# Kernel tuning notes

Hardware: AMD Instinct MI355X
Metric: run time of the kernel (lower is better)

Reference implementation:

```python
import jax, jax.numpy as jnp
import numpy as np

B, L, DIM = 2, 2048, 768
NH, HD = 12, 64  # num_heads, head_dim; NH*HD == dim_attn == 768


def setup_inputs() -> dict:
    key = jax.random.key(0)
    ks = jax.random.split(key, 7)
    x = jax.random.normal(ks[0], (B, L, DIM), dtype=jnp.float32)
    pos_bias = jax.random.normal(ks[1], (1, NH, L, L), dtype=jnp.float32)
    Wq = jax.random.normal(ks[2], (DIM, DIM), dtype=jnp.float32) * 0.02
    Wk = jax.random.normal(ks[3], (DIM, DIM), dtype=jnp.float32) * 0.02
    Wv = jax.random.normal(ks[4], (DIM, DIM), dtype=jnp.float32) * 0.02
    Wo = jax.random.normal(ks[5], (DIM, DIM), dtype=jnp.float32) * 0.02
    mask = jax.random.randint(ks[6], (B, L), 0, 2, dtype=jnp.int32)
    return {"x": x, "pos_bias": pos_bias, "Wq": Wq, "Wk": Wk, "Wv": Wv,
            "Wo": Wo, "mask": mask}


def reference(x, pos_bias, Wq, Wk, Wv, Wo, mask):
    b, l, _ = x.shape
    # q/k/v projections (torch Linear: x @ W.T), split into heads
    q = (x @ Wq.T).reshape(b, l, NH, HD)
    k = (x @ Wk.T).reshape(b, l, NH, HD)
    v = (x @ Wv.T).reshape(b, l, NH, HD)
    # additive bias [B, H, Lq, Lk]: pos_bias broadcast + key mask -> -inf
    neg_inf = jnp.finfo(x.dtype).min
    attn_bias = jnp.broadcast_to(pos_bias, (b, NH, l, l))
    attn_bias = jnp.where(mask[:, None, None, :] == 0, neg_inf, attn_bias)
    # T5-style attention: NO 1/sqrt(d) scaling
    scores = jnp.einsum('binc,bjnc->bnij', q, k) + attn_bias
    attn = jax.nn.softmax(scores.astype(jnp.float32), axis=-1).astype(x.dtype)
    out = jnp.einsum('bnij,bjnc->binc', attn, v).reshape(b, l, NH * HD)
    return out @ Wo.T
```

## Files before the change

kernel.cpp:

```cpp
#include <hip/hip_runtime.h>
#include <math.h>

#define Bq 2
#define Lq 2048
#define DIMq 768
#define NHq 12
#define HDq 64
#define LOG2E 1.44269504f

typedef __attribute__((ext_vector_type(8))) short short8;
typedef __attribute__((ext_vector_type(4))) short short4v;
typedef __attribute__((ext_vector_type(4))) float float4v;

typedef __attribute__((address_space(3))) unsigned int as3_u32;
typedef __attribute__((address_space(1))) unsigned int as1_u32;

static __device__ __forceinline__ short f2bf(float f) {
    union { float f; unsigned u; } v; v.f = f;
    unsigned r = (v.u + 0x7FFF + ((v.u >> 16) & 1)) >> 16;
    return (short)r;
}

static __device__ __forceinline__ void gld_lds16(const short* g, short* l) {
    __builtin_amdgcn_global_load_lds((const as1_u32*)g, (as3_u32*)l, 16, 0, 0);
}

__global__ __launch_bounds__(256)
void to_bf16(const float* __restrict__ x,  const float* __restrict__ wq,
             const float* __restrict__ wk, const float* __restrict__ wv,
             const float* __restrict__ wo,
             short* __restrict__ xb, short* __restrict__ wqb,
             short* __restrict__ wkb, short* __restrict__ wvb,
             short* __restrict__ wob)
{
    int blk = blockIdx.x;
    const float* s; short* d; int off;
    if      (blk <  768) { s = x;  d = xb;  off = blk * 1024; }
    else if (blk <  912) { s = wq; d = wqb; off = (blk -  768) * 1024; }
    else if (blk < 1056) { s = wk; d = wkb; off = (blk -  912) * 1024; }
    else if (blk < 1200) { s = wv; d = wvb; off = (blk - 1056) * 1024; }
    else                 { s = wo; d = wob; off = (blk - 1200) * 1024; }
    const float4* s4 = (const float4*)s;
    short4v* d4 = (short4v*)d;
#pragma unroll
    for (int i = 0; i < 4; ++i) {
        int idx = off + threadIdx.x + i * 256;
        float4 v = s4[idx];
        short4v o;
        o[0] = f2bf(v.x); o[1] = f2bf(v.y); o[2] = f2bf(v.z); o[3] = f2bf(v.w);
        d4[idx] = o;
    }
}

__global__ __launch_bounds__(256, 2)
void gemm_bf16(const short* __restrict__ A,
               const short* __restrict__ W0, const short* __restrict__ W1,
               const short* __restrict__ W2,
               short* __restrict__ D0, short* __restrict__ D1,
               short* __restrict__ D2, float* __restrict__ DF, int mode)
{
    const int z = blockIdx.z;
    const short* W = (z == 0) ? W0 : ((z == 1) ? W1 : W2);
    short* DH = (z == 0) ? D0 : ((z == 1) ? D1 : D2);

    __shared__ __align__(16) short As[128][64];
    __shared__ __align__(16) short Ws[128][64];

    const int tid  = threadIdx.x;
    const int wave = tid >> 6;
    const int lane = tid & 63;
    const int col  = lane & 15;
    const int quad = lane >> 4;
    const int wr = wave >> 1, wc = wave & 1;
    const int m0 = blockIdx.y * 128, n0 = blockIdx.x * 128;

    float4v acc[4][4];
#pragma unroll
    for (int mt = 0; mt < 4; ++mt)
#pragma unroll
        for (int nt = 0; nt < 4; ++nt) acc[mt][nt] = (float4v){0.f, 0.f, 0.f, 0.f};

    const short* Ab = A + (size_t)m0 * DIMq;
    const short* Wb = W + (size_t)n0 * DIMq;

    for (int k0 = 0; k0 < DIMq; k0 += 64) {
        __syncthreads();
#pragma unroll
        for (int i = 0; i < 4; ++i) {
            int g = i * 256 + tid;
            int row = g >> 3, ch = g & 7;
            gld_lds16(Ab + (size_t)row * DIMq + k0 + ch * 8, (short*)As + g * 8);
            gld_lds16(Wb + (size_t)row * DIMq + k0 + ch * 8, (short*)Ws + g * 8);
        }
        __syncthreads();
#pragma unroll
        for (int kk = 0; kk < 2; ++kk) {
            short8 a[4], bfr[4];
#pragma unroll
            for (int mt = 0; mt < 4; ++mt)
                a[mt] = *(const short8*)&As[wr * 64 + mt * 16 + col][kk * 32 + quad * 8];
#pragma unroll
            for (int nt = 0; nt < 4; ++nt)
                bfr[nt] = *(const short8*)&Ws[wc * 64 + nt * 16 + col][kk * 32 + quad * 8];
#pragma unroll
            for (int mt = 0; mt < 4; ++mt)
#pragma unroll
                for (int nt = 0; nt < 4; ++nt)
                    acc[mt][nt] = __builtin_amdgcn_mfma_f32_16x16x32_bf16(
                        a[mt], bfr[nt], acc[mt][nt], 0, 0, 0);
        }
    }

#pragma unroll
    for (int mt = 0; mt < 4; ++mt)
#pragma unroll
    for (int reg = 0; reg < 4; ++reg) {
        int m = m0 + wr * 64 + mt * 16 + quad * 4 + reg;
#pragma unroll
        for (int nt = 0; nt < 4; ++nt) {
            int n = n0 + wc * 64 + nt * 16 + col;
            if (mode == 1) {
                int b = m >> 11, l = m & 2047, h = n >> 6, c = n & 63;
                DH[(((size_t)(b * NHq + h)) * Lq + l) * HDq + c] = f2bf(acc[mt][nt][reg]);
            } else {
                DF[(size_t)m * DIMq + n] = acc[mt][nt][reg];
            }
        }
    }
}

__global__ __launch_bounds__(256)
void transpose_v(const short* __restrict__ Vh, short* __restrict__ VT)
{
    const int lt = blockIdx.x;
    const int bh = blockIdx.y;
    const short* src = Vh + ((size_t)bh * Lq + lt * 64) * HDq;
    short* dst = VT + (size_t)bh * HDq * Lq + lt * 64;
    __shared__ __align__(16) short t[64][72];
    const int tid = threadIdx.x;
    {
        int row = tid & 63, seg = tid >> 6;
        *(short8*)&t[row][seg * 16]     = *(const short8*)&src[row * HDq + seg * 16];
        *(short8*)&t[row][seg * 16 + 8] = *(const short8*)&src[row * HDq + seg * 16 + 8];
    }
    __syncthreads();
    {
        int c = tid >> 2, seg = tid & 3;
        short8 o0, o1;
#pragma unroll
        for (int j = 0; j < 8; ++j) o0[j] = t[seg * 16 + j][c];
#pragma unroll
        for (int j = 0; j < 8; ++j) o1[j] = t[seg * 16 + 8 + j][c];
        *(short8*)&dst[(size_t)c * Lq + seg * 16]     = o0;
        *(short8*)&dst[(size_t)c * Lq + seg * 16 + 8] = o1;
    }
}

__global__ __launch_bounds__(256, 2)
void attn_fwd_mfma(const short* __restrict__ Qh, const short* __restrict__ Kh,
                   const short* __restrict__ VT, const float* __restrict__ pos_bias,
                   const int* __restrict__ mask, short* __restrict__ AO)
{
    const int hw = blockIdx.x;
    const int logical = (hw & 7) * 96 + (hw >> 3);
    const int b  = logical & 1;
    const int qt = (logical >> 1) & 31;
    const int h  = logical >> 6;

    const short* Q = Qh + ((size_t)(b * NHq + h)) * Lq * HDq;
    const short* K = Kh + ((size_t)(b * NHq + h)) * Lq * HDq;
    const short* V = VT + ((size_t)(b * NHq + h)) * HDq * Lq;
    const int* mk = mask + (size_t)b * Lq;

    __shared__ __align__(16) short Ks[2][64][72];
    __shared__ __align__(16) short Vt[2][64][72];
    __shared__ __align__(16) short Ps[64][72];

    const int tid  = threadIdx.x;
    const int wave = tid >> 6;
    const int lane = tid & 63;
    const int col  = lane & 15;
    const int quad = lane >> 4;

    short8 qa[2];
    {
        const short* qrow = Q + (size_t)(qt * 64 + wave * 16 + col) * HDq;
        qa[0] = *(const short8*)&qrow[quad * 8];
        qa[1] = *(const short8*)&qrow[32 + quad * 8];
    }

    const float* brow = pos_bias + (size_t)h * Lq * Lq
                      + (size_t)(qt * 64 + wave * 16 + quad * 4) * Lq + col;

    float bcur[4][4], bnxt[4][4];
    auto prefetch = [&](int kt, float (&bb)[4][4]) {
#pragma unroll
        for (int nt = 0; nt < 4; ++nt) {
            int mval = mk[kt * 64 + col + 16 * nt];
            float fm = (mval == 0) ? -1e30f : 0.0f;
#pragma unroll
            for (int reg = 0; reg < 4; ++reg)
                bb[nt][reg] = (brow[(size_t)reg * Lq + kt * 64 + 16 * nt] + fm) * LOG2E;
        }
    };

    short8 kreg[2], vreg[2];
    auto loadKV = [&](int kt) {
        const short* Kt = K + (size_t)kt * 64 * HDq;
#pragma unroll
        for (int i = 0; i < 2; ++i) {
            int idx = tid + i * 256;
            kreg[i] = *(const short8*)&Kt[(idx >> 3) * HDq + (idx & 7) * 8];
            vreg[i] = *(const short8*)&V[(size_t)(idx >> 3) * Lq + kt * 64 + (idx & 7) * 8];
        }
    };
    auto writeKV = [&](int buf) {
#pragma unroll
        for (int i = 0; i < 2; ++i) {
            int idx = tid + i * 256;
            *(short8*)&Ks[buf][idx >> 3][(idx & 7) * 8] = kreg[i];
            *(short8*)&Vt[buf][idx >> 3][(idx & 7) * 8] = vreg[i];
        }
    };

    float4v Oacc[4];
    float l_part[4];
#pragma unroll
    for (int nt = 0; nt < 4; ++nt) Oacc[nt] = (float4v){0.f, 0.f, 0.f, 0.f};
#pragma unroll
    for (int r = 0; r < 4; ++r) l_part[r] = 0.f;

    loadKV(0);
    writeKV(0);
    prefetch(0, bcur);
    __syncthreads();

    int cur = 0;
    for (int kt = 0; kt < Lq / 64; ++kt) {
        const bool more = (kt + 1 < Lq / 64);
        if (more) {
            loadKV(kt + 1);
            prefetch(kt + 1, bnxt);
        }

        float4v S[4];
#pragma unroll
        for (int nt = 0; nt < 4; ++nt) S[nt] = (float4v){0.f, 0.f, 0.f, 0.f};
        __builtin_amdgcn_s_setprio(1);
#pragma unroll
        for (int kk = 0; kk < 2; ++kk) {
#pragma unroll
            for (int nt = 0; nt < 4; ++nt) {
                short8 bfr = *(const short8*)&Ks[cur][nt * 16 + col][kk * 32 + quad * 8];
                S[nt] = __builtin_amdgcn_mfma_f32_16x16x32_bf16(qa[kk], bfr, S[nt], 0, 0, 0);
            }
        }
        __builtin_amdgcn_s_setprio(0);

#pragma unroll
        for (int nt = 0; nt < 4; ++nt)
#pragma unroll
            for (int reg = 0; reg < 4; ++reg) {
                float p = __builtin_amdgcn_exp2f(
                    __builtin_fmaf(S[nt][reg], LOG2E, bcur[nt][reg]));
                l_part[reg] += p;
                Ps[wave * 16 + quad * 4 + reg][col + 16 * nt] = f2bf(p);
            }

        __builtin_amdgcn_s_setprio(1);
#pragma unroll
        for (int kk = 0; kk < 2; ++kk) {
            short8 pa = *(const short8*)&Ps[wave * 16 + col][kk * 32 + quad * 8];
#pragma unroll
            for (int nt = 0; nt < 4; ++nt) {
                short8 vb = *(const short8*)&Vt[cur][nt * 16 + col][kk * 32 + quad * 8];
                Oacc[nt] = __builtin_amdgcn_mfma_f32_16x16x32_bf16(pa, vb, Oacc[nt], 0, 0, 0);
            }
        }
        __builtin_amdgcn_s_setprio(0);

        if (more) writeKV(cur ^ 1);
        __syncthreads();
        cur ^= 1;

#pragma unroll
        for (int nt = 0; nt < 4; ++nt)
#pragma unroll
            for (int reg = 0; reg < 4; ++reg)
                bcur[nt][reg] = bnxt[nt][reg];
    }

    float l[4];
#pragma unroll
    for (int reg = 0; reg < 4; ++reg) {
        float s = l_part[reg];
#pragma unroll
        for (int off = 1; off < 16; off <<= 1)
            s += __shfl_xor(s, off, 64);
        l[reg] = s;
    }

    short* aorow = AO + ((size_t)b * Lq + qt * 64 + wave * 16 + quad * 4) * DIMq
                 + h * HDq + col;
#pragma unroll
    for (int reg = 0; reg < 4; ++reg) {
        float inv = 1.0f / l[reg];
#pragma unroll
        for (int nt = 0; nt < 4; ++nt)
            aorow[(size_t)reg * DIMq + 16 * nt] = f2bf(Oacc[nt][reg] * inv);
    }
}

extern "C" void kernel_launch(void* const* d_in, const int* in_sizes, int n_in,
                              void* d_out, int out_size, void* d_ws, size_t ws_size,
                              hipStream_t stream) {
    const float* x        = (const float*)d_in[0];
    const float* pos_bias = (const float*)d_in[1];
    const float* Wq       = (const float*)d_in[2];
    const float* Wk       = (const float*)d_in[3];
    const float* Wv       = (const float*)d_in[4];
    const float* Wo       = (const float*)d_in[5];
    const int*   mask     = (const int*)d_in[6];
    float* out = (float*)d_out;

    const size_t nX = (size_t)Bq * Lq * DIMq;
    const size_t nW = (size_t)DIMq * DIMq;
    short* xb  = (short*)d_ws;
    short* wqb = xb  + nX;
    short* wkb = wqb + nW;
    short* wvb = wkb + nW;
    short* wob = wvb + nW;
    short* Qh  = wob + nW;
    short* Kh  = Qh  + nX;
    short* Vh  = Kh  + nX;
    short* AOb = Vh  + nX;
    short* VTb = xb;

    dim3 blk(256);
    hipLaunchKernelGGL(to_bf16, dim3(1344), blk, 0, stream,
                       x, Wq, Wk, Wv, Wo, xb, wqb, wkb, wvb, wob);

    hipLaunchKernelGGL(gemm_bf16, dim3(DIMq / 128, (Bq * Lq) / 128, 3), blk, 0, stream,
                       xb, wqb, wkb, wvb, Qh, Kh, Vh, (float*)nullptr, 1);

    hipLaunchKernelGGL(transpose_v, dim3(Lq / 64, Bq * NHq), blk, 0, stream,
                       Vh, VTb);

    hipLaunchKernelGGL(attn_fwd_mfma, dim3(Lq / 64 * NHq * Bq), blk, 0, stream,
                       Qh, Kh, VTb, pos_bias, mask, AOb);

    hipLaunchKernelGGL(gemm_bf16, dim3(DIMq / 128, (Bq * Lq) / 128, 1), blk, 0, stream,
                       AOb, wob, wob, wob, (short*)nullptr, (short*)nullptr,
                       (short*)nullptr, out, 0);
}
```

Measured before the change: 388.1 us.

## Split attention over key dimension and swizzle LDS tiles to avoid bank conflicts

The attention kernel now splits the key sequence into two halves, doubling the grid to 1536 blocks. Each block writes unnormalized fp32 partial outputs and row sums, and a new combine kernel adds the halves, normalizes and converts to bf16. This works without a running max because the kernel uses no max subtraction. The LDS tiles also drop padding in favour of an XOR swizzle, to reduce bank conflicts and shared memory use. The split raises parallelism and occupancy, at the cost of an extra launch and extra fp32 global traffic for the partials.

Result: slower. 400.4 us (+3.2%).

```diff
diff --git a/kernel.cpp b/kernel.cpp
--- a/kernel.cpp
+++ b/kernel.cpp
@@ -7,6 +7,8 @@
 #define NHq 12
 #define HDq 64
 #define LOG2E 1.44269504f
+#define NSPLIT 2
+#define KT_PER_SPLIT (Lq / 64 / NSPLIT)
 
 typedef __attribute__((ext_vector_type(8))) short short8;
 typedef __attribute__((ext_vector_type(4))) short short4v;
@@ -159,22 +161,24 @@
 __global__ __launch_bounds__(256, 2)
 void attn_fwd_mfma(const short* __restrict__ Qh, const short* __restrict__ Kh,
                    const short* __restrict__ VT, const float* __restrict__ pos_bias,
-                   const int* __restrict__ mask, short* __restrict__ AO)
+                   const int* __restrict__ mask,
+                   float* __restrict__ Op, float* __restrict__ Lp)
 {
     const int hw = blockIdx.x;
-    const int logical = (hw & 7) * 96 + (hw >> 3);
-    const int b  = logical & 1;
-    const int qt = (logical >> 1) & 31;
-    const int h  = logical >> 6;
+    const int logical = (hw & 7) * 192 + (hw >> 3);
+    const int s  = logical & 1;
+    const int b  = (logical >> 1) & 1;
+    const int qt = (logical >> 2) & 31;
+    const int h  = logical >> 7;
 
     const short* Q = Qh + ((size_t)(b * NHq + h)) * Lq * HDq;
     const short* K = Kh + ((size_t)(b * NHq + h)) * Lq * HDq;
     const short* V = VT + ((size_t)(b * NHq + h)) * HDq * Lq;
     const int* mk = mask + (size_t)b * Lq;
 
-    __shared__ __align__(16) short Ks[2][64][72];
-    __shared__ __align__(16) short Vt[2][64][72];
-    __shared__ __align__(16) short Ps[64][72];
+    __shared__ __align__(16) short Ks[2][64][64];
+    __shared__ __align__(16) short Vt[2][64][64];
+    __shared__ __align__(16) short Ps[64][64];
 
     const int tid  = threadIdx.x;
     const int wave = tid >> 6;
@@ -182,6 +186,9 @@
     const int col  = lane & 15;
     const int quad = lane >> 4;
 
+    const int ktbeg = s * KT_PER_SPLIT;
+    const int ktend = ktbeg + KT_PER_SPLIT;
+
     short8 qa[2];
     {
         const short* qrow = Q + (size_t)(qt * 64 + wave * 16 + col) * HDq;
@@ -218,8 +225,10 @@
 #pragma unroll
         for (int i = 0; i < 2; ++i) {
             int idx = tid + i * 256;
-            *(short8*)&Ks[buf][idx >> 3][(idx & 7) * 8] = kreg[i];
-            *(short8*)&Vt[buf][idx >> 3][(idx & 7) * 8] = vreg[i];
+            int row = idx >> 3;
+            int ofs = ((idx & 7) * 16) ^ ((row & 7) << 4);
+            *(short8*)((char*)&Ks[buf][0][0] + row * 128 + ofs) = kreg[i];
+            *(short8*)((char*)&Vt[buf][0][0] + row * 128 + ofs) = vreg[i];
         }
     };
 
@@ -230,19 +239,20 @@
 #pragma unroll
     for (int r = 0; r < 4; ++r) l_part[r] = 0.f;
 
-    loadKV(0);
+    loadKV(ktbeg);
     writeKV(0);
-    prefetch(0, bcur);
+    prefetch(ktbeg, bcur);
     __syncthreads();
 
     int cur = 0;
-    for (int kt = 0; kt < Lq / 64; ++kt) {
-        const bool more = (kt + 1 < Lq / 64);
+    for (int kt = ktbeg; kt < ktend; ++kt) {
+        const bool more = (kt + 1 < ktend);
         if (more) {
             loadKV(kt + 1);
             prefetch(kt + 1, bnxt);
         }
 
+        const int rofs = (col & 7) << 4;
         float4v S[4];
 #pragma unroll
         for (int nt = 0; nt < 4; ++nt) S[nt] = (float4v){0.f, 0.f, 0.f, 0.f};
@@ -251,7 +261,8 @@
         for (int kk = 0; kk < 2; ++kk) {
 #pragma unroll
             for (int nt = 0; nt < 4; ++nt) {
-                short8 bfr = *(const short8*)&Ks[cur][nt * 16 + col][kk * 32 + quad * 8];
+                short8 bfr = *(const short8*)((const char*)&Ks[cur][0][0]
+                              + (nt * 16 + col) * 128 + ((kk * 64 + quad * 16) ^ rofs));
                 S[nt] = __builtin_amdgcn_mfma_f32_16x16x32_bf16(qa[kk], bfr, S[nt], 0, 0, 0);
             }
         }
@@ -264,16 +275,20 @@
                 float p = __builtin_amdgcn_exp2f(
                     __builtin_fmaf(S[nt][reg], LOG2E, bcur[nt][reg]));
                 l_part[reg] += p;
-                Ps[wave * 16 + quad * 4 + reg][col + 16 * nt] = f2bf(p);
+                int prow = wave * 16 + quad * 4 + reg;
+                *(short*)((char*)&Ps[0][0] + prow * 128
+                          + (((col + 16 * nt) * 2) ^ ((prow & 7) << 4))) = f2bf(p);
             }
 
         __builtin_amdgcn_s_setprio(1);
 #pragma unroll
         for (int kk = 0; kk < 2; ++kk) {
-            short8 pa = *(const short8*)&Ps[wave * 16 + col][kk * 32 + quad * 8];
+            short8 pa = *(const short8*)((const char*)&Ps[0][0]
+                          + (wave * 16 + col) * 128 + ((kk * 64 + quad * 16) ^ rofs));
 #pragma unroll
             for (int nt = 0; nt < 4; ++nt) {
-                short8 vb = *(const short8*)&Vt[cur][nt * 16 + col][kk * 32 + quad * 8];
+                short8 vb = *(const short8*)((const char*)&Vt[cur][0][0]
+                              + (nt * 16 + col) * 128 + ((kk * 64 + quad * 16) ^ rofs));
                 Oacc[nt] = __builtin_amdgcn_mfma_f32_16x16x32_bf16(pa, vb, Oacc[nt], 0, 0, 0);
             }
         }
@@ -293,22 +308,52 @@
     float l[4];
 #pragma unroll
     for (int reg = 0; reg < 4; ++reg) {
-        float s = l_part[reg];
+        float v = l_part[reg];
 #pragma unroll
         for (int off = 1; off < 16; off <<= 1)
-            s += __shfl_xor(s, off, 64);
-        l[reg] = s;
-    }
-
-    short* aorow = AO + ((size_t)b * Lq + qt * 64 + wave * 16 + quad * 4) * DIMq
-                 + h * HDq + col;
-#pragma unroll
-    for (int reg = 0; reg < 4; ++reg) {
-        float inv = 1.0f / l[reg];
+            v += __shfl_xor(v, off, 64);
+        l[reg] = v;
+    }
+
+    float* orow = Op + (((size_t)(s * Bq + b)) * Lq + qt * 64 + wave * 16 + quad * 4) * DIMq
+                + h * HDq + col;
+#pragma unroll
+    for (int reg = 0; reg < 4; ++reg)
 #pragma unroll
         for (int nt = 0; nt < 4; ++nt)
-            aorow[(size_t)reg * DIMq + 16 * nt] = f2bf(Oacc[nt][reg] * inv);
-    }
+            orow[(size_t)reg * DIMq + 16 * nt] = Oacc[nt][reg];
+
+    if (col == 0) {
+        float* lrow = Lp + (((size_t)(s * Bq + b)) * NHq + h) * Lq
+                    + qt * 64 + wave * 16 + quad * 4;
+#pragma unroll
+        for (int reg = 0; reg < 4; ++reg) lrow[reg] = l[reg];
+    }
+}
+
+__global__ __launch_bounds__(256)
+void combine_split(const float* __restrict__ Op, const float* __restrict__ Lp,
+                   short* __restrict__ AO)
+{
+    const int idx = blockIdx.x * 256 + threadIdx.x;
+    const int row = idx / (DIMq / 4);
+    const int d4  = idx - row * (DIMq / 4);
+    const int h   = d4 >> 4;
+    const int b   = row >> 11, l = row & 2047;
+
+    const float4* O0 = (const float4*)Op;
+    const float4* O1 = O0 + (size_t)Bq * Lq * (DIMq / 4);
+    float l0 = Lp[((size_t)b * NHq + h) * Lq + l];
+    float l1 = Lp[(((size_t)Bq + b) * NHq + h) * Lq + l];
+    float inv = 1.0f / (l0 + l1);
+
+    float4 a = O0[idx], c = O1[idx];
+    short4v o;
+    o[0] = f2bf((a.x + c.x) * inv);
+    o[1] = f2bf((a.y + c.y) * inv);
+    o[2] = f2bf((a.z + c.z) * inv);
+    o[3] = f2bf((a.w + c.w) * inv);
+    ((short4v*)AO)[idx] = o;
 }
 
 extern "C" void kernel_launch(void* const* d_in, const int* in_sizes, int n_in,
@@ -334,6 +379,8 @@
     short* Kh  = Qh  + nX;
     short* Vh  = Kh  + nX;
     short* AOb = Vh  + nX;
+    float* Opf = (float*)(AOb + nX);
+    float* Lpf = Opf + (size_t)NSPLIT * nX;
     short* VTb = xb;
 
     dim3 blk(256);
@@ -346,8 +393,11 @@
     hipLaunchKernelGGL(transpose_v, dim3(Lq / 64, Bq * NHq), blk, 0, stream,
                        Vh, VTb);
 
-    hipLaunchKernelGGL(attn_fwd_mfma, dim3(Lq / 64 * NHq * Bq), blk, 0, stream,
-                       Qh, Kh, VTb, pos_bias, mask, AOb);
+    hipLaunchKernelGGL(attn_fwd_mfma, dim3(Lq / 64 * NHq * Bq * NSPLIT), blk, 0, stream,
+                       Qh, Kh, VTb, pos_bias, mask, Opf, Lpf);
+
+    hipLaunchKernelGGL(combine_split, dim3(nX / 4 / 256), blk, 0, stream,
+                       Opf, Lpf, AOb);
 
     hipLaunchKernelGGL(gemm_bf16, dim3(DIMq / 128, (Bq * Lq) / 128, 1), blk, 0, stream,
                        AOb, wob, wob, wob, (short*)nullptr, (short*)nullptr,
```

## Split attention key tiles across wave pairs with 512-thread blocks

Applied to the files above, without the earlier changes.

The attention kernel now runs 8 waves per block instead of 4. Each pair of waves shares a 16-row query slice and splits the 64-key tile (and the 64 output columns) in half, so each wave does half the MFMAs and half the bias loads. The goal is more parallelism and latency hiding for the bias streaming that dominates the kernel. This adds an extra __syncthreads per iteration, because P is written by both waves before the PV step, and a shared-memory exchange to combine the row sums at the end. Launch bounds rise to 512 threads with 6 blocks per CU, which caps registers per thread.

Result: no change. 384.1 us (-1.0%).

```diff
diff --git a/kernel.cpp b/kernel.cpp
--- a/kernel.cpp
+++ b/kernel.cpp
@@ -156,7 +156,7 @@
     }
 }
 
-__global__ __launch_bounds__(256, 2)
+__global__ __launch_bounds__(512, 6)
 void attn_fwd_mfma(const short* __restrict__ Qh, const short* __restrict__ Kh,
                    const short* __restrict__ VT, const float* __restrict__ pos_bias,
                    const int* __restrict__ mask, short* __restrict__ AO)
@@ -175,58 +175,55 @@
     __shared__ __align__(16) short Ks[2][64][72];
     __shared__ __align__(16) short Vt[2][64][72];
     __shared__ __align__(16) short Ps[64][72];
+    __shared__ float lbuf[8][16];
 
     const int tid  = threadIdx.x;
     const int wave = tid >> 6;
     const int lane = tid & 63;
     const int col  = lane & 15;
     const int quad = lane >> 4;
+    const int wrow = wave >> 1;
+    const int wkey = wave & 1;
 
     short8 qa[2];
     {
-        const short* qrow = Q + (size_t)(qt * 64 + wave * 16 + col) * HDq;
+        const short* qrow = Q + (size_t)(qt * 64 + wrow * 16 + col) * HDq;
         qa[0] = *(const short8*)&qrow[quad * 8];
         qa[1] = *(const short8*)&qrow[32 + quad * 8];
     }
 
     const float* brow = pos_bias + (size_t)h * Lq * Lq
-                      + (size_t)(qt * 64 + wave * 16 + quad * 4) * Lq + col;
-
-    float bcur[4][4], bnxt[4][4];
-    auto prefetch = [&](int kt, float (&bb)[4][4]) {
-#pragma unroll
-        for (int nt = 0; nt < 4; ++nt) {
-            int mval = mk[kt * 64 + col + 16 * nt];
+                      + (size_t)(qt * 64 + wrow * 16 + quad * 4) * Lq + col;
+
+    float bcur[2][4], bnxt[2][4];
+    auto prefetch = [&](int kt, float (&bb)[2][4]) {
+#pragma unroll
+        for (int ntl = 0; ntl < 2; ++ntl) {
+            int nt = wkey * 2 + ntl;
+            int mval = mk[kt * 64 + nt * 16 + col];
             float fm = (mval == 0) ? -1e30f : 0.0f;
 #pragma unroll
             for (int reg = 0; reg < 4; ++reg)
-                bb[nt][reg] = (brow[(size_t)reg * Lq + kt * 64 + 16 * nt] + fm) * LOG2E;
+                bb[ntl][reg] = (brow[(size_t)reg * Lq + kt * 64 + nt * 16] + fm) * LOG2E;
         }
     };
 
-    short8 kreg[2], vreg[2];
+    short8 kreg, vreg;
     auto loadKV = [&](int kt) {
-        const short* Kt = K + (size_t)kt * 64 * HDq;
-#pragma unroll
-        for (int i = 0; i < 2; ++i) {
-            int idx = tid + i * 256;
-            kreg[i] = *(const short8*)&Kt[(idx >> 3) * HDq + (idx & 7) * 8];
-            vreg[i] = *(const short8*)&V[(size_t)(idx >> 3) * Lq + kt * 64 + (idx & 7) * 8];
-        }
+        int row = tid >> 3, ch = tid & 7;
+        kreg = *(const short8*)&K[(size_t)(kt * 64 + row) * HDq + ch * 8];
+        vreg = *(const short8*)&V[(size_t)row * Lq + kt * 64 + ch * 8];
     };
     auto writeKV = [&](int buf) {
-#pragma unroll
-        for (int i = 0; i < 2; ++i) {
-            int idx = tid + i * 256;
-            *(short8*)&Ks[buf][idx >> 3][(idx & 7) * 8] = kreg[i];
-            *(short8*)&Vt[buf][idx >> 3][(idx & 7) * 8] = vreg[i];
-        }
+        int row = tid >> 3, ch = tid & 7;
+        *(short8*)&Ks[buf][row][ch * 8] = kreg;
+        *(short8*)&Vt[buf][row][ch * 8] = vreg;
     };
 
-    float4v Oacc[4];
+    float4v Oacc[2];
     float l_part[4];
 #pragma unroll
-    for (int nt = 0; nt < 4; ++nt) Oacc[nt] = (float4v){0.f, 0.f, 0.f, 0.f};
+    for (int ntl = 0; ntl < 2; ++ntl) Oacc[ntl] = (float4v){0.f, 0.f, 0.f, 0.f};
 #pragma unroll
     for (int r = 0; r < 4; ++r) l_part[r] = 0.f;
 
@@ -243,38 +240,41 @@
             prefetch(kt + 1, bnxt);
         }
 
-        float4v S[4];
-#pragma unroll
-        for (int nt = 0; nt < 4; ++nt) S[nt] = (float4v){0.f, 0.f, 0.f, 0.f};
+        float4v S[2];
+#pragma unroll
+        for (int ntl = 0; ntl < 2; ++ntl) S[ntl] = (float4v){0.f, 0.f, 0.f, 0.f};
         __builtin_amdgcn_s_setprio(1);
 #pragma unroll
         for (int kk = 0; kk < 2; ++kk) {
 #pragma unroll
-            for (int nt = 0; nt < 4; ++nt) {
-                short8 bfr = *(const short8*)&Ks[cur][nt * 16 + col][kk * 32 + quad * 8];
-                S[nt] = __builtin_amdgcn_mfma_f32_16x16x32_bf16(qa[kk], bfr, S[nt], 0, 0, 0);
+            for (int ntl = 0; ntl < 2; ++ntl) {
+                short8 bfr = *(const short8*)
+                    &Ks[cur][(wkey * 2 + ntl) * 16 + col][kk * 32 + quad * 8];
+                S[ntl] = __builtin_amdgcn_mfma_f32_16x16x32_bf16(qa[kk], bfr, S[ntl], 0, 0, 0);
             }
         }
         __builtin_amdgcn_s_setprio(0);
 
 #pragma unroll
-        for (int nt = 0; nt < 4; ++nt)
+        for (int ntl = 0; ntl < 2; ++ntl)
 #pragma unroll
             for (int reg = 0; reg < 4; ++reg) {
                 float p = __builtin_amdgcn_exp2f(
-                    __builtin_fmaf(S[nt][reg], LOG2E, bcur[nt][reg]));
+                    __builtin_fmaf(S[ntl][reg], LOG2E, bcur[ntl][reg]));
                 l_part[reg] += p;
-                Ps[wave * 16 + quad * 4 + reg][col + 16 * nt] = f2bf(p);
+                Ps[wrow * 16 + quad * 4 + reg][(wkey * 2 + ntl) * 16 + col] = f2bf(p);
             }
+        __syncthreads();
 
         __builtin_amdgcn_s_setprio(1);
 #pragma unroll
         for (int kk = 0; kk < 2; ++kk) {
-            short8 pa = *(const short8*)&Ps[wave * 16 + col][kk * 32 + quad * 8];
-#pragma unroll
-            for (int nt = 0; nt < 4; ++nt) {
-                short8 vb = *(const short8*)&Vt[cur][nt * 16 + col][kk * 32 + quad * 8];
-                Oacc[nt] = __builtin_amdgcn_mfma_f32_16x16x32_bf16(pa, vb, Oacc[nt], 0, 0, 0);
+            short8 pa = *(const short8*)&Ps[wrow * 16 + col][kk * 32 + quad * 8];
+#pragma unroll
+            for (int ntl = 0; ntl < 2; ++ntl) {
+                short8 vb = *(const short8*)
+                    &Vt[cur][(wkey * 2 + ntl) * 16 + col][kk * 32 + quad * 8];
+                Oacc[ntl] = __builtin_amdgcn_mfma_f32_16x16x32_bf16(pa, vb, Oacc[ntl], 0, 0, 0);
             }
         }
         __builtin_amdgcn_s_setprio(0);
@@ -284,30 +284,36 @@
         cur ^= 1;
 
 #pragma unroll
-        for (int nt = 0; nt < 4; ++nt)
+        for (int ntl = 0; ntl < 2; ++ntl)
 #pragma unroll
             for (int reg = 0; reg < 4; ++reg)
-                bcur[nt][reg] = bnxt[nt][reg];
-    }
-
-    float l[4];
+                bcur[ntl][reg] = bnxt[ntl][reg];
+    }
+
+    float lown[4];
 #pragma unroll
     for (int reg = 0; reg < 4; ++reg) {
-        float s = l_part[reg];
+        float v = l_part[reg];
 #pragma unroll
         for (int off = 1; off < 16; off <<= 1)
-            s += __shfl_xor(s, off, 64);
-        l[reg] = s;
-    }
-
-    short* aorow = AO + ((size_t)b * Lq + qt * 64 + wave * 16 + quad * 4) * DIMq
-                 + h * HDq + col;
+            v += __shfl_xor(v, off, 64);
+        lown[reg] = v;
+    }
+    if (col == 0) {
+#pragma unroll
+        for (int reg = 0; reg < 4; ++reg)
+            lbuf[wave][quad * 4 + reg] = lown[reg];
+    }
+    __syncthreads();
+
+    short* aorow = AO + ((size_t)b * Lq + qt * 64 + wrow * 16 + quad * 4) * DIMq
+                 + h * HDq + wkey * 32 + col;
 #pragma unroll
     for (int reg = 0; reg < 4; ++reg) {
-        float inv = 1.0f / l[reg];
-#pragma unroll
-        for (int nt = 0; nt < 4; ++nt)
-            aorow[(size_t)reg * DIMq + 16 * nt] = f2bf(Oacc[nt][reg] * inv);
+        float inv = 1.0f / (lown[reg] + lbuf[wave ^ 1][quad * 4 + reg]);
+#pragma unroll
+        for (int ntl = 0; ntl < 2; ++ntl)
+            aorow[(size_t)reg * DIMq + 16 * ntl] = f2bf(Oacc[ntl][reg] * inv);
     }
 }
 
@@ -346,7 +352,7 @@
     hipLaunchKernelGGL(transpose_v, dim3(Lq / 64, Bq * NHq), blk, 0, stream,
                        Vh, VTb);
 
-    hipLaunchKernelGGL(attn_fwd_mfma, dim3(Lq / 64 * NHq * Bq), blk, 0, stream,
+    hipLaunchKernelGGL(attn_fwd_mfma, dim3(Lq / 64 * NHq * Bq), dim3(512), 0, stream,
                        Qh, Kh, VTb, pos_bias, mask, AOb);
 
     hipLaunchKernelGGL(gemm_bf16, dim3(DIMq / 128, (Bq * Lq) / 128, 1), blk, 0, stream,
```
